# Performance work log

Measured on AMD Instinct MI355X. Metric: run time of the kernel, lower is better.

Reference implementation:

```python
import jax, jax.numpy as jnp
import numpy as np

B, T, C = 2, 1024, 1024
H, D = 16, 64
E, I = 16, 256
EPS = 1e-5


def _ln(x, g, b):
    mu = x.mean(-1, keepdims=True)
    var = ((x - mu) ** 2).mean(-1, keepdims=True)
    return (x - mu) * jax.lax.rsqrt(var + EPS) * g + b


def setup_inputs() -> dict:
    key = jax.random.key(0)
    ks = jax.random.split(key, 10)
    s = 0.02
    return {
        "hidden_states": jax.random.normal(ks[0], (B, T, C), jnp.float32),
        "ln1_g": jnp.ones((C,), jnp.float32), "ln1_b": jnp.zeros((C,), jnp.float32),
        "ln2_g": jnp.ones((C,), jnp.float32), "ln2_b": jnp.zeros((C,), jnp.float32),
        "wq": jax.random.normal(ks[1], (C, C), jnp.float32) * s,
        "wk": jax.random.normal(ks[2], (C, C), jnp.float32) * s,
        "wv": jax.random.normal(ks[3], (C, C), jnp.float32) * s,
        "wo": jax.random.normal(ks[4], (C, C), jnp.float32) * s,
        "sim_matrix": jax.random.normal(ks[5], (C, E), jnp.float32),
        "threshold": jnp.zeros((1,), jnp.float32),
        "w1": jax.random.normal(ks[6], (E, C, I), jnp.float32) * s,
        "w2": jax.random.normal(ks[7], (E, I, C), jnp.float32) * s,
    }


def reference(hidden_states, ln1_g, ln1_b, ln2_g, ln2_b, wq, wk, wv, wo,
              sim_matrix, threshold, w1, w2):
    x = hidden_states
    # ---- attention (causal SDPA) ----
    h = _ln(x, ln1_g, ln1_b)
    q = (h @ wq).reshape(B, T, H, D)
    k = (h @ wk).reshape(B, T, H, D)
    v = (h @ wv).reshape(B, T, H, D)
    logits = jnp.einsum('bqhd,bkhd->bhqk', q, k) / np.float32(np.sqrt(D))
    causal = jnp.tril(jnp.ones((T, T), bool))
    logits = jnp.where(causal, logits, jnp.float32(-1e9))
    attn = jax.nn.softmax(logits, axis=-1)
    ao = jnp.einsum('bhqk,bkhd->bqhd', attn, v).reshape(B, T, C) @ wo
    x = x + ao
    # ---- MoE ----
    h2 = _ln(x, ln2_g, ln2_b).reshape(-1, C)          # [N, C]
    xn = h2 / jnp.linalg.norm(h2, axis=-1, keepdims=True)
    wn = sim_matrix / jnp.linalg.norm(sim_matrix, axis=0, keepdims=True)
    scores = xn @ wn                                   # [N, E]
    mask = scores > threshold                          # bool [N, E]
    k_per_token = mask.sum(-1)
    # dense expert compute; zero out non-activated slots (matches index_put buffer)
    mid = jax.nn.gelu(jnp.einsum('nc,eci->nei', h2, w1), approximate=False)
    expert_outputs_full = jnp.einsum('nei,eic->nec', mid, w2) * mask[:, :, None].astype(jnp.float32)
    # STE gate: value == mask, gradient flows to scores as identity
    ste = scores + jax.lax.stop_gradient(mask.astype(jnp.float32) - scores)
    final = (expert_outputs_full * ste[:, :, None]).sum(1).reshape(B, T, C)
    x = x + final
    return (x, scores, expert_outputs_full, k_per_token)
```

## Files before the change

kernel.cpp:

```cpp
#include <hip/hip_runtime.h>
#include <hip/hip_bf16.h>
#include <math.h>

#define BB 2
#define TT 1024
#define CC 1024
#define HH 16
#define DD 64
#define EE 16
#define II 256
#define NN (BB*TT)
#define EPSLN 1e-5f
#define LDA 72

typedef __attribute__((ext_vector_type(8))) short short8;
typedef __attribute__((ext_vector_type(4))) short s16x4;
typedef __attribute__((ext_vector_type(4))) float f32x4;

__device__ inline void splitbf(float x, short& hi, short& lo) {
    __hip_bfloat16 h = __float2bfloat16(x);
    float hf = __bfloat162float(h);
    __hip_bfloat16 l = __float2bfloat16(x - hf);
    hi = *(short*)&h;
    lo = *(short*)&l;
}

__global__ __launch_bounds__(256) void ln_kernel(const float* __restrict__ x,
                                                 const float* __restrict__ g,
                                                 const float* __restrict__ bta,
                                                 float* __restrict__ out,
                                                 __hip_bfloat16* __restrict__ outb,
                                                 __hip_bfloat16* __restrict__ outh,
                                                 __hip_bfloat16* __restrict__ outl) {
    const int row = blockIdx.x, tid = threadIdx.x;
    __shared__ float r1[256], r2[256];
    const float* xr = x + (long)row * CC;
    float4 xv = ((const float4*)xr)[tid];
    float s  = xv.x + xv.y + xv.z + xv.w;
    float q2 = xv.x*xv.x + xv.y*xv.y + xv.z*xv.z + xv.w*xv.w;
    r1[tid] = s; r2[tid] = q2; __syncthreads();
    for (int st = 128; st > 0; st >>= 1) {
        if (tid < st) { r1[tid] += r1[tid+st]; r2[tid] += r2[tid+st]; }
        __syncthreads();
    }
    const float mu  = r1[0] * (1.f/CC);
    const float var = r2[0] * (1.f/CC) - mu*mu;
    const float rs  = rsqrtf(var + EPSLN);
    float4 gv = ((const float4*)g)[tid];
    float4 bv = ((const float4*)bta)[tid];
    float4 ov;
    ov.x = (xv.x-mu)*rs*gv.x + bv.x;
    ov.y = (xv.y-mu)*rs*gv.y + bv.y;
    ov.z = (xv.z-mu)*rs*gv.z + bv.z;
    ov.w = (xv.w-mu)*rs*gv.w + bv.w;
    if (out)
        ((float4*)(out + (long)row * CC))[tid] = ov;
    if (outb) {
        __hip_bfloat16* p = outb + (long)row * CC + tid*4;
        p[0] = __float2bfloat16(ov.x); p[1] = __float2bfloat16(ov.y);
        p[2] = __float2bfloat16(ov.z); p[3] = __float2bfloat16(ov.w);
    }
    if (outh) {
        float xs[4] = {ov.x, ov.y, ov.z, ov.w};
        s16x4 hv, lv;
        #pragma unroll
        for (int j = 0; j < 4; j++) { short h,l; splitbf(xs[j], h, l); hv[j]=h; lv[j]=l; }
        *(s16x4*)(outh + (long)row * CC + tid*4) = hv;
        *(s16x4*)(outl + (long)row * CC + tid*4) = lv;
    }
}

__global__ __launch_bounds__(256) void transpose_split(const float* __restrict__ W,
                                                       __hip_bfloat16* __restrict__ Wth,
                                                       __hip_bfloat16* __restrict__ Wtl,
                                                       int K, int N) {
    const int n0 = blockIdx.x * 32, k0 = blockIdx.y * 32;
    __shared__ float t[32][33];
    const int tx = threadIdx.x & 31, ty = threadIdx.x >> 5;
    #pragma unroll
    for (int i = 0; i < 4; i++)
        t[ty + i*8][tx] = W[(long)(k0 + ty + i*8)*N + n0 + tx];
    __syncthreads();
    #pragma unroll
    for (int i = 0; i < 4; i++) {
        float v = t[tx][ty + i*8];
        short h, l; splitbf(v, h, l);
        *(short*)&Wth[(long)(n0 + ty + i*8)*K + k0 + tx] = h;
        *(short*)&Wtl[(long)(n0 + ty + i*8)*K + k0 + tx] = l;
    }
}

__global__ __launch_bounds__(256) void transpose_v_bf16(
        const __hip_bfloat16* __restrict__ Vh, const __hip_bfloat16* __restrict__ Vl,
        __hip_bfloat16* __restrict__ Vth, __hip_bfloat16* __restrict__ Vtl) {
    const int b = blockIdx.z;
    const int c0 = blockIdx.y * 32, t0 = blockIdx.x * 32;
    __shared__ unsigned short th[32][33], tl[32][33];
    const int tx = threadIdx.x & 31, ty = threadIdx.x >> 5;
    const unsigned short* vh = (const unsigned short*)Vh;
    const unsigned short* vl = (const unsigned short*)Vl;
    #pragma unroll
    for (int i = 0; i < 4; i++) {
        const long src = ((long)b*TT + t0 + ty + i*8)*CC + c0 + tx;
        th[ty + i*8][tx] = vh[src];
        tl[ty + i*8][tx] = vl[src];
    }
    __syncthreads();
    #pragma unroll
    for (int i = 0; i < 4; i++) {
        const int gc = c0 + ty + i*8;
        const int hh = gc >> 6, d = gc & 63;
        const long dst = ((long)(b*HH + hh)*64 + d)*TT + t0 + tx;
        ((unsigned short*)Vth)[dst] = th[tx][ty + i*8];
        ((unsigned short*)Vtl)[dst] = tl[tx][ty + i*8];
    }
}

template<int EPI>
__global__ __launch_bounds__(256, 2) void gemm_split(
        const __hip_bfloat16* __restrict__ Ah,
        const __hip_bfloat16* __restrict__ Al,
        const __hip_bfloat16* __restrict__ Bh_base,
        const __hip_bfloat16* __restrict__ Bl_base,
        float* __restrict__ C_base,
        __hip_bfloat16* __restrict__ Ch_base,
        __hip_bfloat16* __restrict__ Cl_base,
        int M, int N, int K,
        const float* __restrict__ resid) {
    __shared__ __hip_bfloat16 Ash[64][40], Asl[64][40];
    __shared__ __hip_bfloat16 Bsh[128][40], Bsl[128][40];
    const int z = blockIdx.z;
    const __hip_bfloat16* Bth = Bh_base + (long)z * N * K;
    const __hip_bfloat16* Btl = Bl_base + (long)z * N * K;
    const int n0 = blockIdx.x * 128, m0 = blockIdx.y * 64;
    const int tid = threadIdx.x;
    const int wave = tid >> 6, lane = tid & 63;
    const int wm = (wave >> 1) * 32, wn = (wave & 1) * 64;
    const int l15 = lane & 15, quad = lane >> 4;

    f32x4 acc[2][4] = {};

    for (int k0 = 0; k0 < K; k0 += 32) {
        {
            const int r = tid >> 2, kg = (tid & 3) * 8;
            *(short8*)&Ash[r][kg] = *(const short8*)(Ah + (long)(m0 + r)*K + k0 + kg);
            *(short8*)&Asl[r][kg] = *(const short8*)(Al + (long)(m0 + r)*K + k0 + kg);
        }
        #pragma unroll
        for (int it = 0; it < 2; it++) {
            const int idx = tid + it*256;
            const int r = idx >> 2, kg = (idx & 3) * 8;
            *(short8*)&Bsh[r][kg] = *(const short8*)(Bth + (long)(n0 + r)*K + k0 + kg);
            *(short8*)&Bsl[r][kg] = *(const short8*)(Btl + (long)(n0 + r)*K + k0 + kg);
        }
        __syncthreads();
        short8 ah[2], al[2], bh[4], bl[4];
        #pragma unroll
        for (int mi = 0; mi < 2; mi++) {
            ah[mi] = *(const short8*)&Ash[wm + mi*16 + l15][quad*8];
            al[mi] = *(const short8*)&Asl[wm + mi*16 + l15][quad*8];
        }
        #pragma unroll
        for (int ni = 0; ni < 4; ni++) {
            bh[ni] = *(const short8*)&Bsh[wn + ni*16 + l15][quad*8];
            bl[ni] = *(const short8*)&Bsl[wn + ni*16 + l15][quad*8];
        }
        #pragma unroll
        for (int mi = 0; mi < 2; mi++)
            #pragma unroll
            for (int ni = 0; ni < 4; ni++) {
                acc[mi][ni] = __builtin_amdgcn_mfma_f32_16x16x32_bf16(ah[mi], bh[ni], acc[mi][ni], 0,0,0);
                acc[mi][ni] = __builtin_amdgcn_mfma_f32_16x16x32_bf16(ah[mi], bl[ni], acc[mi][ni], 0,0,0);
                acc[mi][ni] = __builtin_amdgcn_mfma_f32_16x16x32_bf16(al[mi], bh[ni], acc[mi][ni], 0,0,0);
            }
        __syncthreads();
    }

    #pragma unroll
    for (int mi = 0; mi < 2; mi++)
        #pragma unroll
        for (int r = 0; r < 4; r++) {
            const int row = m0 + wm + mi*16 + quad*4 + r;
            #pragma unroll
            for (int ni = 0; ni < 4; ni++) {
                const int col = n0 + wn + ni*16 + l15;
                float val = acc[mi][ni][r];
                if (EPI == 2) {
                    short hh, ll; splitbf(val, hh, ll);
                    *(short*)&Ch_base[(long)z*M*N + (long)row*N + col] = hh;
                    *(short*)&Cl_base[(long)z*M*N + (long)row*N + col] = ll;
                } else {
                    if (EPI == 1) val += resid[(long)row*N + col];
                    C_base[(long)z*M*N + (long)row*N + col] = val;
                }
            }
        }
}

template<int EPI>
__global__ __launch_bounds__(256) void gemm_mfma(
        const __hip_bfloat16* __restrict__ A, long sAe,
        const __hip_bfloat16* __restrict__ Bt, long sBe,
        void* __restrict__ Cp, long sCe, int ldc,
        int M, int N, int K,
        const float* __restrict__ mask) {
    constexpr int LDK = 40;
    __shared__ __hip_bfloat16 As[128][LDK];
    __shared__ __hip_bfloat16 Bs[128][LDK];
    const int e = blockIdx.z;
    A  += (long)e * sAe;
    Bt += (long)e * sBe;
    const int n0 = blockIdx.x * 128, m0 = blockIdx.y * 128;
    const int tid = threadIdx.x;
    const int wave = tid >> 6, lane = tid & 63;
    const int wm = (wave >> 1) * 64, wn = (wave & 1) * 64;
    const int l15 = lane & 15, quad = lane >> 4;

    f32x4 acc[4][4] = {};

    for (int k0 = 0; k0 < K; k0 += 32) {
        #pragma unroll
        for (int it = 0; it < 2; it++) {
            int idx = tid + it*256;
            int r = idx >> 2, kg = idx & 3;
            short8 av = *(const short8*)(A  + (long)(m0 + r)*K + k0 + kg*8);
            short8 bv = *(const short8*)(Bt + (long)(n0 + r)*K + k0 + kg*8);
            *(short8*)&As[r][kg*8] = av;
            *(short8*)&Bs[r][kg*8] = bv;
        }
        __syncthreads();
        short8 af[4], bff[4];
        #pragma unroll
        for (int i = 0; i < 4; i++) {
            af[i]  = *(const short8*)&As[wm + i*16 + l15][quad*8];
            bff[i] = *(const short8*)&Bs[wn + i*16 + l15][quad*8];
        }
        #pragma unroll
        for (int mi = 0; mi < 4; mi++)
            #pragma unroll
            for (int ni = 0; ni < 4; ni++)
                acc[mi][ni] = __builtin_amdgcn_mfma_f32_16x16x32_bf16(
                                  af[mi], bff[ni], acc[mi][ni], 0, 0, 0);
        __syncthreads();
    }

    #pragma unroll
    for (int mi = 0; mi < 4; mi++) {
        #pragma unroll
        for (int r = 0; r < 4; r++) {
            const int row = m0 + wm + mi*16 + quad*4 + r;
            float mv = 0.f;
            if (EPI == 1) mv = mask[(long)row*EE + e];
            #pragma unroll
            for (int ni = 0; ni < 4; ni++) {
                const int col = n0 + wn + ni*16 + l15;
                float val = acc[mi][ni][r];
                if (EPI == 0) {
                    val = 0.5f*val*(1.f + erff(val*0.70710678118f));
                    ((__hip_bfloat16*)Cp)[(long)e*sCe + (long)row*ldc + col] =
                        __float2bfloat16(val);
                } else {
                    ((float*)Cp)[(long)e*sCe + (long)row*ldc + col] = val*mv;
                }
            }
        }
    }
}

__global__ __launch_bounds__(256) void transpose_f2b(const float* __restrict__ W, long sWe,
                                                     __hip_bfloat16* __restrict__ Wt, long sWte,
                                                     int K, int N) {
    const int e = blockIdx.z;
    W  += (long)e * sWe;
    Wt += (long)e * sWte;
    const int n0 = blockIdx.x * 32, k0 = blockIdx.y * 32;
    __shared__ float t[32][33];
    const int tx = threadIdx.x & 31, ty = threadIdx.x >> 5;
    #pragma unroll
    for (int i = 0; i < 4; i++)
        t[ty + i*8][tx] = W[(long)(k0 + ty + i*8)*N + n0 + tx];
    __syncthreads();
    #pragma unroll
    for (int i = 0; i < 4; i++)
        Wt[(long)(n0 + ty + i*8)*K + k0 + tx] = __float2bfloat16(t[tx][ty + i*8]);
}

__global__ __launch_bounds__(256, 4) void attn_split(
        const __hip_bfloat16* __restrict__ Qh, const __hip_bfloat16* __restrict__ Ql,
        const __hip_bfloat16* __restrict__ Kh, const __hip_bfloat16* __restrict__ Kl,
        const __hip_bfloat16* __restrict__ Vtg_h, const __hip_bfloat16* __restrict__ Vtg_l,
        float* __restrict__ Opart,
        float* __restrict__ mpart,
        float* __restrict__ lpart) {
    __shared__ __hip_bfloat16 KPh[64][LDA], KPl[64][LDA];
    __shared__ __hip_bfloat16 Vth[64][LDA], Vtl[64][LDA];

    const int bx = blockIdx.x;
    const int qt = 15 - (bx >> 1), half = bx & 1;
    const int h = blockIdx.y, b = blockIdx.z;
    const int tid = threadIdx.x;
    const int wave = tid >> 6, lane = tid & 63;
    const int l15 = lane & 15, quad = lane >> 4;
    const int wm = wave * 16;
    const long tbase = (long)b * TT * CC + (long)h * DD;
    const long vbase = (long)(b*HH + h) * 64 * TT;
    const int pidx = ((b*HH + h)*16 + qt)*2 + half;
    float* Op = Opart + (long)pidx * 4096;

    const int n_kt = qt + 1, mid_kt = (n_kt + 1) >> 1;
    const int kt_lo = half ? mid_kt : 0;
    const int kt_hi = half ? n_kt   : mid_kt;

    if (kt_lo >= kt_hi) {
        for (int i = tid; i < 64*64; i += 256) Op[i] = 0.f;
        if (tid < 64) { mpart[(long)pidx*64 + tid] = -1e30f; lpart[(long)pidx*64 + tid] = 0.f; }
        return;
    }

    short8 qh[2], ql[2];
    {
        const long qoff = tbase + (long)(qt*64 + wm + l15)*CC;
        #pragma unroll
        for (int kc = 0; kc < 2; kc++) {
            qh[kc] = *(const short8*)(Qh + qoff + kc*32 + quad*8);
            ql[kc] = *(const short8*)(Ql + qoff + kc*32 + quad*8);
        }
    }

    f32x4 oacc[4] = {};
    float m_run[4], l_run[4];
    #pragma unroll
    for (int r = 0; r < 4; r++) { m_run[r] = -1e30f; l_run[r] = 0.f; }

    for (int kt = kt_lo; kt < kt_hi; kt++) {
        __syncthreads();
        #pragma unroll
        for (int it = 0; it < 2; it++) {
            const int idx = tid + it*256;
            const int r = idx >> 3, g = (idx & 7)*8;
            const long koff = tbase + (long)(kt*64 + r)*CC + g;
            const long voff = vbase + (long)r*TT + kt*64 + g;
            *(short8*)&KPh[r][g] = *(const short8*)(Kh + koff);
            *(short8*)&KPl[r][g] = *(const short8*)(Kl + koff);
            *(short8*)&Vth[r][g] = *(const short8*)(Vtg_h + voff);
            *(short8*)&Vtl[r][g] = *(const short8*)(Vtg_l + voff);
        }
        __syncthreads();

        f32x4 s[4] = {};
        #pragma unroll
        for (int nt = 0; nt < 4; nt++)
            #pragma unroll
            for (int kc = 0; kc < 2; kc++) {
                short8 bh = *(const short8*)&KPh[nt*16 + l15][kc*32 + quad*8];
                short8 bl = *(const short8*)&KPl[nt*16 + l15][kc*32 + quad*8];
                s[nt] = __builtin_amdgcn_mfma_f32_16x16x32_bf16(qh[kc], bh, s[nt], 0,0,0);
                s[nt] = __builtin_amdgcn_mfma_f32_16x16x32_bf16(qh[kc], bl, s[nt], 0,0,0);
                s[nt] = __builtin_amdgcn_mfma_f32_16x16x32_bf16(ql[kc], bh, s[nt], 0,0,0);
            }

        const bool diag = (kt == qt);
        float alpha[4];
        float pr[4][4];
        #pragma unroll
        for (int r = 0; r < 4; r++) {
            const int rowg = wm + quad*4 + r;
            float sv[4], mx = -1e30f;
            #pragma unroll
            for (int nt = 0; nt < 4; nt++) {
                float val = s[nt][r] * 0.125f;
                if (diag && (nt*16 + l15) > rowg) val = -1e30f;
                sv[nt] = val;
                mx = fmaxf(mx, val);
            }
            #pragma unroll
            for (int off = 1; off < 16; off <<= 1) mx = fmaxf(mx, __shfl_xor(mx, off, 16));
            const float mnew = fmaxf(m_run[r], mx);
            alpha[r] = __expf(m_run[r] - mnew);
            float rs = 0.f;
            #pragma unroll
            for (int nt = 0; nt < 4; nt++) {
                float p = __expf(sv[nt] - mnew);
                pr[r][nt] = p;
                rs += p;
            }
            #pragma unroll
            for (int off = 1; off < 16; off <<= 1) rs += __shfl_xor(rs, off, 16);
            l_run[r] = l_run[r]*alpha[r] + rs;
            m_run[r] = mnew;
        }
        __syncthreads();

        #pragma unroll
        for (int r = 0; r < 4; r++)
            #pragma unroll
            for (int nt = 0; nt < 4; nt++) {
                short hh, ll; splitbf(pr[r][nt], hh, ll);
                *(short*)&KPh[wm + quad*4 + r][nt*16 + l15] = hh;
                *(short*)&KPl[wm + quad*4 + r][nt*16 + l15] = ll;
            }

        #pragma unroll
        for (int dt = 0; dt < 4; dt++)
            #pragma unroll
            for (int r = 0; r < 4; r++)
                oacc[dt][r] *= alpha[r];
        #pragma unroll
        for (int kc = 0; kc < 2; kc++) {
            short8 ph = *(const short8*)&KPh[wm + l15][kc*32 + quad*8];
            short8 pl = *(const short8*)&KPl[wm + l15][kc*32 + quad*8];
            #pragma unroll
            for (int dt = 0; dt < 4; dt++) {
                short8 vh = *(const short8*)&Vth[dt*16 + l15][kc*32 + quad*8];
                short8 vl = *(const short8*)&Vtl[dt*16 + l15][kc*32 + quad*8];
                oacc[dt] = __builtin_amdgcn_mfma_f32_16x16x32_bf16(ph, vh, oacc[dt], 0,0,0);
                oacc[dt] = __builtin_amdgcn_mfma_f32_16x16x32_bf16(ph, vl, oacc[dt], 0,0,0);
                oacc[dt] = __builtin_amdgcn_mfma_f32_16x16x32_bf16(pl, vh, oacc[dt], 0,0,0);
            }
        }
    }

    #pragma unroll
    for (int dt = 0; dt < 4; dt++)
        #pragma unroll
        for (int r = 0; r < 4; r++)
            Op[(wm + quad*4 + r)*64 + dt*16 + l15] = oacc[dt][r];
    if (l15 == 0) {
        #pragma unroll
        for (int r = 0; r < 4; r++) {
            mpart[(long)pidx*64 + wm + quad*4 + r] = m_run[r];
            lpart[(long)pidx*64 + wm + quad*4 + r] = l_run[r];
        }
    }
}

__global__ __launch_bounds__(256) void attn_merge(const float* __restrict__ Opart,
                                                  const float* __restrict__ mpart,
                                                  const float* __restrict__ lpart,
                                                  __hip_bfloat16* __restrict__ aoh,
                                                  __hip_bfloat16* __restrict__ aol) {
    const int qt = blockIdx.x, h = blockIdx.y, b = blockIdx.z;
    const int pA = ((b*HH + h)*16 + qt)*2, pB = pA + 1;
    const int tid = threadIdx.x;
    const int r = tid >> 2, c0 = (tid & 3) * 16;
    const float mA = mpart[(long)pA*64 + r], mB = mpart[(long)pB*64 + r];
    const float lA = lpart[(long)pA*64 + r], lB = lpart[(long)pB*64 + r];
    const float M  = fmaxf(mA, mB);
    const float wA = __expf(mA - M), wB = __expf(mB - M);
    const float inv = 1.f / (lA*wA + lB*wB);
    const float* OA = Opart + (long)pA*4096 + r*64 + c0;
    const float* OB = Opart + (long)pB*4096 + r*64 + c0;
    const long dst = (long)b*TT*CC + (long)(qt*64 + r)*CC + h*DD + c0;
    #pragma unroll
    for (int j = 0; j < 16; j += 4) {
        float4 oa = *(const float4*)(OA + j);
        float4 ob = *(const float4*)(OB + j);
        float o0 = (oa.x*wA + ob.x*wB)*inv;
        float o1 = (oa.y*wA + ob.y*wB)*inv;
        float o2 = (oa.z*wA + ob.z*wB)*inv;
        float o3 = (oa.w*wA + ob.w*wB)*inv;
        float xs[4] = {o0, o1, o2, o3};
        s16x4 hv, lv;
        #pragma unroll
        for (int t = 0; t < 4; t++) { short hh,ll; splitbf(xs[t],hh,ll); hv[t]=hh; lv[t]=ll; }
        *(s16x4*)(aoh + dst + j) = hv;
        *(s16x4*)(aol + dst + j) = lv;
    }
}

__global__ __launch_bounds__(256) void colnorm_kernel(const float* __restrict__ sim,
                                                      float* __restrict__ cn) {
    const int e = blockIdx.x, tid = threadIdx.x;
    __shared__ float red[256];
    float s = 0.f;
    for (int c = tid; c < CC; c += 256) {
        float vv = sim[(long)c*EE + e];
        s += vv*vv;
    }
    red[tid] = s; __syncthreads();
    for (int st = 128; st > 0; st >>= 1) {
        if (tid < st) red[tid] += red[tid+st];
        __syncthreads();
    }
    if (tid == 0) cn[e] = sqrtf(red[0]);
}

__global__ __launch_bounds__(256) void scores_kernel(const float* __restrict__ h2,
                                                     const float* __restrict__ sim,
                                                     const float* __restrict__ cn,
                                                     const float* __restrict__ thr,
                                                     float* __restrict__ scores,
                                                     float* __restrict__ kpt,
                                                     float* __restrict__ maskb) {
    const int row = blockIdx.x, tid = threadIdx.x;
    __shared__ float red[256*17];
    float acc[17] = {};
    for (int c = tid; c < CC; c += 256) {
        const float xv = h2[(long)row*CC + c];
        acc[16] += xv*xv;
        const float* sr = sim + (long)c*EE;
        #pragma unroll
        for (int e2 = 0; e2 < EE; e2++) acc[e2] += xv*sr[e2];
    }
    #pragma unroll
    for (int e2 = 0; e2 < 17; e2++) red[tid*17 + e2] = acc[e2];
    __syncthreads();
    for (int st = 128; st > 0; st >>= 1) {
        if (tid < st)
            for (int e2 = 0; e2 < 17; e2++) red[tid*17+e2] += red[(tid+st)*17+e2];
        __syncthreads();
    }
    if (tid < EE) {
        const float nrm = sqrtf(red[16]);
        const float sc  = red[tid] / (nrm * cn[tid]);
        scores[(long)row*EE + tid] = sc;
        const float mkv = sc > thr[0] ? 1.f : 0.f;
        maskb[(long)row*EE + tid] = mkv;
        red[tid] = mkv;
    }
    __syncthreads();
    if (tid == 0) {
        float c2 = 0.f;
        for (int e2 = 0; e2 < EE; e2++) c2 += red[e2];
        kpt[row] = c2;
    }
}

__global__ __launch_bounds__(256) void moe_sum_kernel(const float* __restrict__ eo,
                                                      float* __restrict__ xio) {
    const int row = blockIdx.x, tid = threadIdx.x;
    for (int c = tid; c < CC; c += 256) {
        float s = 0.f;
        #pragma unroll
        for (int e2 = 0; e2 < EE; e2++)
            s += eo[((long)row*EE + e2)*CC + c];
        xio[(long)row*CC + c] += s;
    }
}

extern "C" void kernel_launch(void* const* d_in, const int* in_sizes, int n_in,
                              void* d_out, int out_size, void* d_ws, size_t ws_size,
                              hipStream_t stream) {
    const float* x     = (const float*)d_in[0];
    const float* ln1_g = (const float*)d_in[1];
    const float* ln1_b = (const float*)d_in[2];
    const float* ln2_g = (const float*)d_in[3];
    const float* ln2_b = (const float*)d_in[4];
    const float* wq    = (const float*)d_in[5];
    const float* wk    = (const float*)d_in[6];
    const float* wv    = (const float*)d_in[7];
    const float* wo    = (const float*)d_in[8];
    const float* sim   = (const float*)d_in[9];
    const float* thr   = (const float*)d_in[10];
    const float* w1    = (const float*)d_in[11];
    const float* w2    = (const float*)d_in[12];

    float* out_x      = (float*)d_out;
    float* out_scores = out_x + (long)NN*CC;
    float* out_eo     = out_scores + (long)NN*EE;
    float* out_kpt    = out_eo + (long)NN*EE*CC;

    const long MF = (long)NN*CC;
    const long CK = (long)CC*CC;
    float* ws   = (float*)d_ws;
    float* h = ws;
    __hip_bfloat16* aoh = (__hip_bfloat16*)ws;
    __hip_bfloat16* aol = (__hip_bfloat16*)(ws + MF/2);
    __hip_bfloat16* qkvh = (__hip_bfloat16*)(ws + MF);
    __hip_bfloat16* qkvl = (__hip_bfloat16*)(ws + MF + 3*MF/2);
    __hip_bfloat16* vth = (__hip_bfloat16*)(ws + 4*MF);
    __hip_bfloat16* vtl = (__hip_bfloat16*)(ws + 4*MF + MF/2);
    __hip_bfloat16* h2b = (__hip_bfloat16*)(ws + 5*MF);
    float* Opart = ws + 5*MF + MF/2;
    __hip_bfloat16* hh  = (__hip_bfloat16*)(ws + 5*MF + MF/2);
    __hip_bfloat16* hl  = (__hip_bfloat16*)(ws + 6*MF);
    __hip_bfloat16* mid = (__hip_bfloat16*)(ws + 5*MF + MF/2);
    __hip_bfloat16* wsph = (__hip_bfloat16*)(ws + 7*MF + MF/2);
    __hip_bfloat16* wspl = (__hip_bfloat16*)(ws + 8*MF + MF/2);
    __hip_bfloat16* w1t  = (__hip_bfloat16*)(ws + 7*MF + MF/2);
    __hip_bfloat16* w2t  = (__hip_bfloat16*)(ws + 8*MF + MF/2);
    float* maskb = ws + 9*MF + MF/2;
    float* cn    = maskb + (long)NN*EE;
    float* mpart = cn + 16;
    float* lpart = mpart + 1024L*64;

    {
        dim3 gt(CC/32, CC/32, 1);
        transpose_split<<<gt, 256, 0, stream>>>(wq, wsph + 0*CK, wspl + 0*CK, CC, CC);
        transpose_split<<<gt, 256, 0, stream>>>(wk, wsph + 1*CK, wspl + 1*CK, CC, CC);
        transpose_split<<<gt, 256, 0, stream>>>(wv, wsph + 2*CK, wspl + 2*CK, CC, CC);
        transpose_split<<<gt, 256, 0, stream>>>(wo, wsph + 3*CK, wspl + 3*CK, CC, CC);
    }

    ln_kernel<<<NN, 256, 0, stream>>>(x, ln1_g, ln1_b, nullptr, nullptr, hh, hl);

    {
        dim3 gq(CC/128, NN/64, 3);
        gemm_split<2><<<gq, 256, 0, stream>>>(hh, hl, wsph, wspl,
                                              nullptr, qkvh, qkvl,
                                              NN, CC, CC, nullptr);
    }

    {
        dim3 gv(TT/32, CC/32, BB);
        transpose_v_bf16<<<gv, 256, 0, stream>>>(qkvh + 2*(long)NN*CC, qkvl + 2*(long)NN*CC,
                                                 vth, vtl);
    }

    {
        dim3 gattn(32, HH, BB);
        attn_split<<<gattn, 256, 0, stream>>>(qkvh, qkvl,
                                              qkvh + (long)NN*CC, qkvl + (long)NN*CC,
                                              vth, vtl, Opart, mpart, lpart);
        dim3 gmerge(16, HH, BB);
        attn_merge<<<gmerge, 256, 0, stream>>>(Opart, mpart, lpart, aoh, aol);
    }

    {
        dim3 go(CC/128, NN/64, 1);
        gemm_split<1><<<go, 256, 0, stream>>>(aoh, aol, wsph + 3*CK, wspl + 3*CK,
                                              out_x, nullptr, nullptr,
                                              NN, CC, CC, x);
    }

    {
        dim3 g1(II/32, CC/32, EE);
        transpose_f2b<<<g1, 256, 0, stream>>>(w1, (long)CC*II, w1t, (long)CC*II, CC, II);
        dim3 g2(CC/32, II/32, EE);
        transpose_f2b<<<g2, 256, 0, stream>>>(w2, (long)II*CC, w2t, (long)II*CC, II, CC);
    }

    ln_kernel<<<NN, 256, 0, stream>>>(out_x, ln2_g, ln2_b, h, h2b, nullptr, nullptr);

    colnorm_kernel<<<EE, 256, 0, stream>>>(sim, cn);
    scores_kernel<<<NN, 256, 0, stream>>>(h, sim, cn, thr, out_scores, out_kpt, maskb);

    {
        dim3 g(II/128, NN/128, EE);
        gemm_mfma<0><<<g, 256, 0, stream>>>(h2b, 0, w1t, (long)II*CC,
                                            mid, (long)NN*II, II,
                                            NN, II, CC, nullptr);
    }

    {
        dim3 g(CC/128, NN/128, EE);
        gemm_mfma<1><<<g, 256, 0, stream>>>(mid, (long)NN*II, w2t, (long)II*CC,
                                            out_eo, (long)CC, EE*CC,
                                            NN, CC, II, maskb);
    }

    moe_sum_kernel<<<NN, 256, 0, stream>>>(out_eo, out_x);
}
```

Measured before the change: 477.8 us.

## Fuse LN2 with router and expert reduction into second MoE GEMM

Merges the second layernorm with the router scoring kernel so the fp32 normalized activations are never written and reread. The second expert GEMM now loops over four experts per block, accumulating the masked outputs in registers and atomically adding them into the residual, which removes the separate expert-sum pass over the large expert-output tensor. The four weight transpose launches and the two MoE weight transposes are each merged into one launch. The price is fp32 atomics (nondeterministic summation order) and one quarter as many blocks in the second expert GEMM, which lowers parallelism.

```diff
diff --git a/kernel.cpp b/kernel.cpp
--- a/kernel.cpp
+++ b/kernel.cpp
@@ -28,8 +28,6 @@
 __global__ __launch_bounds__(256) void ln_kernel(const float* __restrict__ x,
                                                  const float* __restrict__ g,
                                                  const float* __restrict__ bta,
-                                                 float* __restrict__ out,
-                                                 __hip_bfloat16* __restrict__ outb,
                                                  __hip_bfloat16* __restrict__ outh,
                                                  __hip_bfloat16* __restrict__ outl) {
     const int row = blockIdx.x, tid = threadIdx.x;
@@ -48,46 +46,133 @@
     const float rs  = rsqrtf(var + EPSLN);
     float4 gv = ((const float4*)g)[tid];
     float4 bv = ((const float4*)bta)[tid];
-    float4 ov;
-    ov.x = (xv.x-mu)*rs*gv.x + bv.x;
-    ov.y = (xv.y-mu)*rs*gv.y + bv.y;
-    ov.z = (xv.z-mu)*rs*gv.z + bv.z;
-    ov.w = (xv.w-mu)*rs*gv.w + bv.w;
-    if (out)
-        ((float4*)(out + (long)row * CC))[tid] = ov;
-    if (outb) {
-        __hip_bfloat16* p = outb + (long)row * CC + tid*4;
-        p[0] = __float2bfloat16(ov.x); p[1] = __float2bfloat16(ov.y);
-        p[2] = __float2bfloat16(ov.z); p[3] = __float2bfloat16(ov.w);
-    }
-    if (outh) {
-        float xs[4] = {ov.x, ov.y, ov.z, ov.w};
-        s16x4 hv, lv;
-        #pragma unroll
-        for (int j = 0; j < 4; j++) { short h,l; splitbf(xs[j], h, l); hv[j]=h; lv[j]=l; }
-        *(s16x4*)(outh + (long)row * CC + tid*4) = hv;
-        *(s16x4*)(outl + (long)row * CC + tid*4) = lv;
-    }
-}
-
-__global__ __launch_bounds__(256) void transpose_split(const float* __restrict__ W,
-                                                       __hip_bfloat16* __restrict__ Wth,
-                                                       __hip_bfloat16* __restrict__ Wtl,
-                                                       int K, int N) {
+    float xs[4];
+    xs[0] = (xv.x-mu)*rs*gv.x + bv.x;
+    xs[1] = (xv.y-mu)*rs*gv.y + bv.y;
+    xs[2] = (xv.z-mu)*rs*gv.z + bv.z;
+    xs[3] = (xv.w-mu)*rs*gv.w + bv.w;
+    s16x4 hv, lv;
+    #pragma unroll
+    for (int j = 0; j < 4; j++) { short h,l; splitbf(xs[j], h, l); hv[j]=h; lv[j]=l; }
+    *(s16x4*)(outh + (long)row * CC + tid*4) = hv;
+    *(s16x4*)(outl + (long)row * CC + tid*4) = lv;
+}
+
+__global__ __launch_bounds__(256) void ln2_router(const float* __restrict__ xio,
+                                                  const float* __restrict__ g,
+                                                  const float* __restrict__ bta,
+                                                  const float* __restrict__ sim,
+                                                  const float* __restrict__ cn,
+                                                  const float* __restrict__ thr,
+                                                  __hip_bfloat16* __restrict__ h2b,
+                                                  float* __restrict__ scores,
+                                                  float* __restrict__ kpt,
+                                                  float* __restrict__ maskb) {
+    const int row = blockIdx.x, tid = threadIdx.x;
+    __shared__ float r1[256], r2[256];
+    __shared__ float red[256*17];
+    float4 xv = ((const float4*)(xio + (long)row*CC))[tid];
+    float s  = xv.x + xv.y + xv.z + xv.w;
+    float q2 = xv.x*xv.x + xv.y*xv.y + xv.z*xv.z + xv.w*xv.w;
+    r1[tid] = s; r2[tid] = q2; __syncthreads();
+    for (int st = 128; st > 0; st >>= 1) {
+        if (tid < st) { r1[tid] += r1[tid+st]; r2[tid] += r2[tid+st]; }
+        __syncthreads();
+    }
+    const float mu  = r1[0] * (1.f/CC);
+    const float var = r2[0] * (1.f/CC) - mu*mu;
+    const float rs  = rsqrtf(var + EPSLN);
+    float4 gv = ((const float4*)g)[tid];
+    float4 bv = ((const float4*)bta)[tid];
+    float ovs[4];
+    ovs[0] = (xv.x-mu)*rs*gv.x + bv.x;
+    ovs[1] = (xv.y-mu)*rs*gv.y + bv.y;
+    ovs[2] = (xv.z-mu)*rs*gv.z + bv.z;
+    ovs[3] = (xv.w-mu)*rs*gv.w + bv.w;
+    {
+        __hip_bfloat16* p = h2b + (long)row*CC + tid*4;
+        p[0] = __float2bfloat16(ovs[0]); p[1] = __float2bfloat16(ovs[1]);
+        p[2] = __float2bfloat16(ovs[2]); p[3] = __float2bfloat16(ovs[3]);
+    }
+    float acc[17] = {};
+    #pragma unroll
+    for (int j = 0; j < 4; j++) {
+        const float v = ovs[j];
+        acc[16] += v*v;
+        const float* sr = sim + (long)(tid*4 + j)*EE;
+        #pragma unroll
+        for (int e2 = 0; e2 < EE; e2++) acc[e2] += v*sr[e2];
+    }
+    #pragma unroll
+    for (int e2 = 0; e2 < 17; e2++) red[tid*17 + e2] = acc[e2];
+    __syncthreads();
+    for (int st = 128; st > 0; st >>= 1) {
+        if (tid < st)
+            for (int e2 = 0; e2 < 17; e2++) red[tid*17+e2] += red[(tid+st)*17+e2];
+        __syncthreads();
+    }
+    if (tid < EE) {
+        const float nrm = sqrtf(red[16]);
+        const float sc  = red[tid] / (nrm * cn[tid]);
+        scores[(long)row*EE + tid] = sc;
+        const float mkv = sc > thr[0] ? 1.f : 0.f;
+        maskb[(long)row*EE + tid] = mkv;
+        red[tid] = mkv;
+    }
+    __syncthreads();
+    if (tid == 0) {
+        float c2 = 0.f;
+        for (int e2 = 0; e2 < EE; e2++) c2 += red[e2];
+        kpt[row] = c2;
+    }
+}
+
+__global__ __launch_bounds__(256) void transpose_split4(const float* __restrict__ W0,
+                                                        const float* __restrict__ W1,
+                                                        const float* __restrict__ W2,
+                                                        const float* __restrict__ W3,
+                                                        __hip_bfloat16* __restrict__ Wth_base,
+                                                        __hip_bfloat16* __restrict__ Wtl_base) {
+    const int z = blockIdx.z;
+    const float* W = (z==0) ? W0 : (z==1) ? W1 : (z==2) ? W2 : W3;
+    __hip_bfloat16* Wth = Wth_base + (long)z*CC*CC;
+    __hip_bfloat16* Wtl = Wtl_base + (long)z*CC*CC;
     const int n0 = blockIdx.x * 32, k0 = blockIdx.y * 32;
     __shared__ float t[32][33];
     const int tx = threadIdx.x & 31, ty = threadIdx.x >> 5;
     #pragma unroll
     for (int i = 0; i < 4; i++)
-        t[ty + i*8][tx] = W[(long)(k0 + ty + i*8)*N + n0 + tx];
+        t[ty + i*8][tx] = W[(long)(k0 + ty + i*8)*CC + n0 + tx];
     __syncthreads();
     #pragma unroll
     for (int i = 0; i < 4; i++) {
         float v = t[tx][ty + i*8];
         short h, l; splitbf(v, h, l);
-        *(short*)&Wth[(long)(n0 + ty + i*8)*K + k0 + tx] = h;
-        *(short*)&Wtl[(long)(n0 + ty + i*8)*K + k0 + tx] = l;
-    }
+        *(short*)&Wth[(long)(n0 + ty + i*8)*CC + k0 + tx] = h;
+        *(short*)&Wtl[(long)(n0 + ty + i*8)*CC + k0 + tx] = l;
+    }
+}
+
+__global__ __launch_bounds__(256) void transpose_f2b_both(const float* __restrict__ w1,
+                                                          const float* __restrict__ w2,
+                                                          __hip_bfloat16* __restrict__ w1t,
+                                                          __hip_bfloat16* __restrict__ w2t) {
+    const int zz = blockIdx.z;
+    const int half = zz >> 4, e = zz & 15;
+    const float* W; __hip_bfloat16* Wt; int K, N, nbx;
+    if (half == 0) { W = w1 + (long)e*CC*II; Wt = w1t + (long)e*CC*II; K = CC; N = II; nbx = II/32; }
+    else           { W = w2 + (long)e*II*CC; Wt = w2t + (long)e*II*CC; K = II; N = CC; nbx = CC/32; }
+    const int bx = blockIdx.x;
+    const int n0 = (bx % nbx) * 32, k0 = (bx / nbx) * 32;
+    __shared__ float t[32][33];
+    const int tx = threadIdx.x & 31, ty = threadIdx.x >> 5;
+    #pragma unroll
+    for (int i = 0; i < 4; i++)
+        t[ty + i*8][tx] = W[(long)(k0 + ty + i*8)*N + n0 + tx];
+    __syncthreads();
+    #pragma unroll
+    for (int i = 0; i < 4; i++)
+        Wt[(long)(n0 + ty + i*8)*K + k0 + tx] = __float2bfloat16(t[tx][ty + i*8]);
 }
 
 __global__ __launch_bounds__(256) void transpose_v_bf16(
@@ -197,18 +282,15 @@
         }
 }
 
-template<int EPI>
-__global__ __launch_bounds__(256) void gemm_mfma(
-        const __hip_bfloat16* __restrict__ A, long sAe,
+__global__ __launch_bounds__(256) void gemm_mfma1(
+        const __hip_bfloat16* __restrict__ A,
         const __hip_bfloat16* __restrict__ Bt, long sBe,
-        void* __restrict__ Cp, long sCe, int ldc,
-        int M, int N, int K,
-        const float* __restrict__ mask) {
+        __hip_bfloat16* __restrict__ Cp, long sCe, int ldc,
+        int M, int N, int K) {
     constexpr int LDK = 40;
     __shared__ __hip_bfloat16 As[128][LDK];
     __shared__ __hip_bfloat16 Bs[128][LDK];
     const int e = blockIdx.z;
-    A  += (long)e * sAe;
     Bt += (long)e * sBe;
     const int n0 = blockIdx.x * 128, m0 = blockIdx.y * 128;
     const int tid = threadIdx.x;
@@ -249,40 +331,93 @@
         #pragma unroll
         for (int r = 0; r < 4; r++) {
             const int row = m0 + wm + mi*16 + quad*4 + r;
-            float mv = 0.f;
-            if (EPI == 1) mv = mask[(long)row*EE + e];
             #pragma unroll
             for (int ni = 0; ni < 4; ni++) {
                 const int col = n0 + wn + ni*16 + l15;
                 float val = acc[mi][ni][r];
-                if (EPI == 0) {
-                    val = 0.5f*val*(1.f + erff(val*0.70710678118f));
-                    ((__hip_bfloat16*)Cp)[(long)e*sCe + (long)row*ldc + col] =
-                        __float2bfloat16(val);
-                } else {
-                    ((float*)Cp)[(long)e*sCe + (long)row*ldc + col] = val*mv;
+                val = 0.5f*val*(1.f + erff(val*0.70710678118f));
+                Cp[(long)e*sCe + (long)row*ldc + col] = __float2bfloat16(val);
+            }
+        }
+    }
+}
+
+__global__ __launch_bounds__(256) void gemm_moe2(
+        const __hip_bfloat16* __restrict__ mid,
+        const __hip_bfloat16* __restrict__ w2t,
+        float* __restrict__ eo,
+        float* __restrict__ xio,
+        const float* __restrict__ mask) {
+    constexpr int LDK = 40;
+    __shared__ __hip_bfloat16 As[128][LDK];
+    __shared__ __hip_bfloat16 Bs[128][LDK];
+    const int e0 = blockIdx.z * 4;
+    const int n0 = blockIdx.x * 128, m0 = blockIdx.y * 128;
+    const int tid = threadIdx.x;
+    const int wave = tid >> 6, lane = tid & 63;
+    const int wm = (wave >> 1) * 64, wn = (wave & 1) * 64;
+    const int l15 = lane & 15, quad = lane >> 4;
+
+    f32x4 sum[4][4] = {};
+
+    for (int ei = 0; ei < 4; ei++) {
+        const int e = e0 + ei;
+        const __hip_bfloat16* A  = mid + (long)e*NN*II;
+        const __hip_bfloat16* Bt = w2t + (long)e*CC*II;
+        f32x4 acc[4][4] = {};
+        for (int k0 = 0; k0 < II; k0 += 32) {
+            #pragma unroll
+            for (int it = 0; it < 2; it++) {
+                int idx = tid + it*256;
+                int r = idx >> 2, kg = idx & 3;
+                short8 av = *(const short8*)(A  + (long)(m0 + r)*II + k0 + kg*8);
+                short8 bv = *(const short8*)(Bt + (long)(n0 + r)*II + k0 + kg*8);
+                *(short8*)&As[r][kg*8] = av;
+                *(short8*)&Bs[r][kg*8] = bv;
+            }
+            __syncthreads();
+            short8 af[4], bff[4];
+            #pragma unroll
+            for (int i = 0; i < 4; i++) {
+                af[i]  = *(const short8*)&As[wm + i*16 + l15][quad*8];
+                bff[i] = *(const short8*)&Bs[wn + i*16 + l15][quad*8];
+            }
+            #pragma unroll
+            for (int mi = 0; mi < 4; mi++)
+                #pragma unroll
+                for (int ni = 0; ni < 4; ni++)
+                    acc[mi][ni] = __builtin_amdgcn_mfma_f32_16x16x32_bf16(
+                                      af[mi], bff[ni], acc[mi][ni], 0, 0, 0);
+            __syncthreads();
+        }
+        #pragma unroll
+        for (int mi = 0; mi < 4; mi++) {
+            #pragma unroll
+            for (int r = 0; r < 4; r++) {
+                const int row = m0 + wm + mi*16 + quad*4 + r;
+                const float mv = mask[(long)row*EE + e];
+                #pragma unroll
+                for (int ni = 0; ni < 4; ni++) {
+                    const int col = n0 + wn + ni*16 + l15;
+                    const float val = acc[mi][ni][r] * mv;
+                    eo[((long)row*EE + e)*CC + col] = val;
+                    sum[mi][ni][r] += val;
                 }
             }
         }
     }
-}
-
-__global__ __launch_bounds__(256) void transpose_f2b(const float* __restrict__ W, long sWe,
-                                                     __hip_bfloat16* __restrict__ Wt, long sWte,
-                                                     int K, int N) {
-    const int e = blockIdx.z;
-    W  += (long)e * sWe;
-    Wt += (long)e * sWte;
-    const int n0 = blockIdx.x * 32, k0 = blockIdx.y * 32;
-    __shared__ float t[32][33];
-    const int tx = threadIdx.x & 31, ty = threadIdx.x >> 5;
-    #pragma unroll
-    for (int i = 0; i < 4; i++)
-        t[ty + i*8][tx] = W[(long)(k0 + ty + i*8)*N + n0 + tx];
-    __syncthreads();
-    #pragma unroll
-    for (int i = 0; i < 4; i++)
-        Wt[(long)(n0 + ty + i*8)*K + k0 + tx] = __float2bfloat16(t[tx][ty + i*8]);
+
+    #pragma unroll
+    for (int mi = 0; mi < 4; mi++)
+        #pragma unroll
+        for (int r = 0; r < 4; r++) {
+            const int row = m0 + wm + mi*16 + quad*4 + r;
+            #pragma unroll
+            for (int ni = 0; ni < 4; ni++) {
+                const int col = n0 + wn + ni*16 + l15;
+                atomicAdd(&xio[(long)row*CC + col], sum[mi][ni][r]);
+            }
+        }
 }
 
 __global__ __launch_bounds__(256, 4) void attn_split(
@@ -455,11 +590,11 @@
     for (int j = 0; j < 16; j += 4) {
         float4 oa = *(const float4*)(OA + j);
         float4 ob = *(const float4*)(OB + j);
-        float o0 = (oa.x*wA + ob.x*wB)*inv;
-        float o1 = (oa.y*wA + ob.y*wB)*inv;
-        float o2 = (oa.z*wA + ob.z*wB)*inv;
-        float o3 = (oa.w*wA + ob.w*wB)*inv;
-        float xs[4] = {o0, o1, o2, o3};
+        float xs[4];
+        xs[0] = (oa.x*wA + ob.x*wB)*inv;
+        xs[1] = (oa.y*wA + ob.y*wB)*inv;
+        xs[2] = (oa.z*wA + ob.z*wB)*inv;
+        xs[3] = (oa.w*wA + ob.w*wB)*inv;
         s16x4 hv, lv;
         #pragma unroll
         for (int t = 0; t < 4; t++) { short hh,ll; splitbf(xs[t],hh,ll); hv[t]=hh; lv[t]=ll; }
@@ -483,59 +618,6 @@
         __syncthreads();
     }
     if (tid == 0) cn[e] = sqrtf(red[0]);
-}
-
-__global__ __launch_bounds__(256) void scores_kernel(const float* __restrict__ h2,
-                                                     const float* __restrict__ sim,
-                                                     const float* __restrict__ cn,
-                                                     const float* __restrict__ thr,
-                                                     float* __restrict__ scores,
-                                                     float* __restrict__ kpt,
-                                                     float* __restrict__ maskb) {
-    const int row = blockIdx.x, tid = threadIdx.x;
-    __shared__ float red[256*17];
-    float acc[17] = {};
-    for (int c = tid; c < CC; c += 256) {
-        const float xv = h2[(long)row*CC + c];
-        acc[16] += xv*xv;
-        const float* sr = sim + (long)c*EE;
-        #pragma unroll
-        for (int e2 = 0; e2 < EE; e2++) acc[e2] += xv*sr[e2];
-    }
-    #pragma unroll
-    for (int e2 = 0; e2 < 17; e2++) red[tid*17 + e2] = acc[e2];
-    __syncthreads();
-    for (int st = 128; st > 0; st >>= 1) {
-        if (tid < st)
-            for (int e2 = 0; e2 < 17; e2++) red[tid*17+e2] += red[(tid+st)*17+e2];
-        __syncthreads();
-    }
-    if (tid < EE) {
-        const float nrm = sqrtf(red[16]);
-        const float sc  = red[tid] / (nrm * cn[tid]);
-        scores[(long)row*EE + tid] = sc;
-        const float mkv = sc > thr[0] ? 1.f : 0.f;
-        maskb[(long)row*EE + tid] = mkv;
-        red[tid] = mkv;
-    }
-    __syncthreads();
-    if (tid == 0) {
-        float c2 = 0.f;
-        for (int e2 = 0; e2 < EE; e2++) c2 += red[e2];
-        kpt[row] = c2;
-    }
-}
-
-__global__ __launch_bounds__(256) void moe_sum_kernel(const float* __restrict__ eo,
-                                                      float* __restrict__ xio) {
-    const int row = blockIdx.x, tid = threadIdx.x;
-    for (int c = tid; c < CC; c += 256) {
-        float s = 0.f;
-        #pragma unroll
-        for (int e2 = 0; e2 < EE; e2++)
-            s += eo[((long)row*EE + e2)*CC + c];
-        xio[(long)row*CC + c] += s;
-    }
 }
 
 extern "C" void kernel_launch(void* const* d_in, const int* in_sizes, int n_in,
@@ -563,7 +645,6 @@
     const long MF = (long)NN*CC;
     const long CK = (long)CC*CC;
     float* ws   = (float*)d_ws;
-    float* h = ws;
     __hip_bfloat16* aoh = (__hip_bfloat16*)ws;
     __hip_bfloat16* aol = (__hip_bfloat16*)(ws + MF/2);
     __hip_bfloat16* qkvh = (__hip_bfloat16*)(ws + MF);
@@ -584,15 +665,14 @@
     float* mpart = cn + 16;
     float* lpart = mpart + 1024L*64;
 
-    {
-        dim3 gt(CC/32, CC/32, 1);
-        transpose_split<<<gt, 256, 0, stream>>>(wq, wsph + 0*CK, wspl + 0*CK, CC, CC);
-        transpose_split<<<gt, 256, 0, stream>>>(wk, wsph + 1*CK, wspl + 1*CK, CC, CC);
-        transpose_split<<<gt, 256, 0, stream>>>(wv, wsph + 2*CK, wspl + 2*CK, CC, CC);
-        transpose_split<<<gt, 256, 0, stream>>>(wo, wsph + 3*CK, wspl + 3*CK, CC, CC);
-    }
-
-    ln_kernel<<<NN, 256, 0, stream>>>(x, ln1_g, ln1_b, nullptr, nullptr, hh, hl);
+    colnorm_kernel<<<EE, 256, 0, stream>>>(sim, cn);
+
+    {
+        dim3 gt(CC/32, CC/32, 4);
+        transpose_split4<<<gt, 256, 0, stream>>>(wq, wk, wv, wo, wsph, wspl);
+    }
+
+    ln_kernel<<<NN, 256, 0, stream>>>(x, ln1_g, ln1_b, hh, hl);
 
     {
         dim3 gq(CC/128, NN/64, 3);
@@ -624,30 +704,22 @@
     }
 
     {
-        dim3 g1(II/32, CC/32, EE);
-        transpose_f2b<<<g1, 256, 0, stream>>>(w1, (long)CC*II, w1t, (long)CC*II, CC, II);
-        dim3 g2(CC/32, II/32, EE);
-        transpose_f2b<<<g2, 256, 0, stream>>>(w2, (long)II*CC, w2t, (long)II*CC, II, CC);
-    }
-
-    ln_kernel<<<NN, 256, 0, stream>>>(out_x, ln2_g, ln2_b, h, h2b, nullptr, nullptr);
-
-    colnorm_kernel<<<EE, 256, 0, stream>>>(sim, cn);
-    scores_kernel<<<NN, 256, 0, stream>>>(h, sim, cn, thr, out_scores, out_kpt, maskb);
+        dim3 ge(256, 1, 2*EE);
+        transpose_f2b_both<<<ge, 256, 0, stream>>>(w1, w2, w1t, w2t);
+    }
+
+    ln2_router<<<NN, 256, 0, stream>>>(out_x, ln2_g, ln2_b, sim, cn, thr,
+                                       h2b, out_scores, out_kpt, maskb);
 
     {
         dim3 g(II/128, NN/128, EE);
-        gemm_mfma<0><<<g, 256, 0, stream>>>(h2b, 0, w1t, (long)II*CC,
-                                            mid, (long)NN*II, II,
-                                            NN, II, CC, nullptr);
-    }
-
-    {
-        dim3 g(CC/128, NN/128, EE);
-        gemm_mfma<1><<<g, 256, 0, stream>>>(mid, (long)NN*II, w2t, (long)II*CC,
-                                            out_eo, (long)CC, EE*CC,
-                                            NN, CC, II, maskb);
-    }
-
-    moe_sum_kernel<<<NN, 256, 0, stream>>>(out_eo, out_x);
-}
+        gemm_mfma1<<<g, 256, 0, stream>>>(h2b, w1t, (long)II*CC,
+                                          mid, (long)NN*II, II,
+                                          NN, II, CC);
+    }
+
+    {
+        dim3 g(CC/128, NN/128, EE/4);
+        gemm_moe2<<<g, 256, 0, stream>>>(mid, w2t, out_eo, out_x, maskb);
+    }
+}
```

New measurement: 486.0 us. Within noise of the previous version (+1.7%).
